# Performance work log

Hardware: AMD Instinct MI355X
Metric: run time of the kernel (lower is better)

The kernel has to match this reference:

```python
import jax, jax.numpy as jnp
import numpy as np

N_NODES = 100000
N_EDGES = 1600000
NUM_GRAPHS = 1000
NODE_IN, EDGE_IN = 32, 16
NODE_EMB, EDGE_EMB, HID, OUT, L = 64, 32, 64, 1, 3
EPS = 1e-5


def _glorot(key, shape):
    fan_in = shape[0]
    return jax.random.normal(key, shape, jnp.float32) / np.sqrt(fan_in)


def setup_inputs() -> dict:
    key = jax.random.key(0)
    ks = jax.random.split(key, 16)
    inp = {
        "x": jax.random.normal(ks[0], (N_NODES, NODE_IN), jnp.float32),
        "edge_attr": jax.random.normal(ks[1], (N_EDGES, EDGE_IN), jnp.float32),
        "edge_index": jax.random.randint(ks[2], (2, N_EDGES), 0, N_NODES, jnp.int64
                                         if jax.config.jax_enable_x64 else jnp.int32),
        "batch": jnp.sort(jax.random.randint(ks[3], (N_NODES,), 0, NUM_GRAPHS)),
        # embeddings
        "node_W": _glorot(ks[4], (NODE_IN, NODE_EMB)),
        "node_b": jnp.zeros((NODE_EMB,), jnp.float32),
        "edge_W": _glorot(ks[5], (EDGE_IN, EDGE_EMB)),
        "edge_b": jnp.zeros((EDGE_EMB,), jnp.float32),
        # per-layer MPNN params (node_dim==64 for every layer since node_emb_dim==hidden_dim)
        "msg_W": _glorot(ks[6], (L, NODE_EMB + EDGE_EMB, HID)),
        "msg_b": jnp.zeros((L, HID), jnp.float32),
        "msg_gamma": jnp.ones((L, HID), jnp.float32),
        "msg_beta": jnp.zeros((L, HID), jnp.float32),
        "upd_W": _glorot(ks[7], (L, NODE_EMB + HID, HID)),
        "upd_b": jnp.zeros((L, HID), jnp.float32),
        "upd_gamma": jnp.ones((L, HID), jnp.float32),
        "upd_beta": jnp.zeros((L, HID), jnp.float32),
        # readout
        "r1_W": _glorot(ks[8], (HID, HID)),
        "r1_b": jnp.zeros((HID,), jnp.float32),
        "r2_W": _glorot(ks[9], (HID, OUT)),
        "r2_b": jnp.zeros((OUT,), jnp.float32),
    }
    return inp


def _bn(h, gamma, beta):
    # BatchNorm1d in training mode: normalize with batch mean / biased variance
    mu = jnp.mean(h, axis=0)
    var = jnp.mean(jnp.square(h - mu), axis=0)
    return gamma * (h - mu) * jax.lax.rsqrt(var + EPS) + beta


def reference(x, edge_attr, edge_index, batch,
              node_W, node_b, edge_W, edge_b,
              msg_W, msg_b, msg_gamma, msg_beta,
              upd_W, upd_b, upd_gamma, upd_beta,
              r1_W, r1_b, r2_W, r2_b):
    h = x @ node_W + node_b                       # [N, 64]
    e = edge_attr @ edge_W + edge_b               # [E, 32]
    src, dst = edge_index[0], edge_index[1]
    for i in range(L):
        # message: gather x_j, concat edge feats, Linear-ReLU-BN (dropout = eval/no-op)
        m = jnp.concatenate([h[src], e], axis=-1) @ msg_W[i] + msg_b[i]   # [E, 64]
        m = _bn(jax.nn.relu(m), msg_gamma[i], msg_beta[i])
        # aggregate: scatter-add to destination nodes
        agg = jax.ops.segment_sum(m, dst, num_segments=N_NODES)          # [N, 64]
        # update: concat self feats, Linear-ReLU-BN
        u = jnp.concatenate([h, agg], axis=-1) @ upd_W[i] + upd_b[i]     # [N, 64]
        h = _bn(jax.nn.relu(u), upd_gamma[i], upd_beta[i])
    # global add pool over graphs
    g = jax.ops.segment_sum(h, batch, num_segments=NUM_GRAPHS)           # [G, 64]
    out = jax.nn.relu(g @ r1_W + r1_b) @ r2_W + r2_b                     # [G, 1]
    return out
```

## Files before the change

kernel.cpp:

```cpp
#include <hip/hip_runtime.h>
#include <hip/hip_bf16.h>

#define N_NODES   100000
#define N_EDGES   1600000
#define NUM_GRAPHS 1000

typedef unsigned int u32;
typedef unsigned short u16;

typedef __bf16 bf16_t;
typedef bf16_t bf16x8 __attribute__((ext_vector_type(8)));
typedef float  f32x4  __attribute__((ext_vector_type(4)));
typedef u32    u32x4  __attribute__((ext_vector_type(4)));

__device__ __forceinline__ float bf2f(u16 u){ return __uint_as_float(((u32)u)<<16); }
__device__ __forceinline__ float BL(u32 u){ return __uint_as_float(u<<16); }
__device__ __forceinline__ float BH(u32 u){ return __uint_as_float(u&0xffff0000u); }
__device__ __forceinline__ u16 f2bf(float f){
  u32 u = __float_as_uint(f);
  return (u16)((u + 0x7fffu + ((u>>16)&1u)) >> 16);
}
__device__ __forceinline__ float ldf(const void* p, size_t i, int isbf){
  return isbf ? bf2f(((const u16*)p)[i]) : ((const float*)p)[i];
}

union U4BF { uint4 u; bf16x8 v; };

__global__ void k_detect(const u32* __restrict__ x, int* __restrict__ flag){
  int t = threadIdx.x; int cnt = 0;
  for (int i = t; i < 256; i += 64){
    u32 w = x[i];
    u32 e = (w >> 7) & 0xffu;
    if (e >= 110u && e <= 137u) cnt++;
  }
  for (int o = 32; o; o >>= 1) cnt += __shfl_xor(cnt, o);
  if (t == 0) *flag = (cnt > 128) ? 1 : 0;
}

__global__ void k_idaff(float* __restrict__ haff){
  int c = threadIdx.x;
  haff[c] = 1.f; haff[64 + c] = 0.f;
}

__global__ void k_prep(const void* __restrict__ eW, const void* __restrict__ eb,
                       const void* __restrict__ mW, const void* __restrict__ mb,
                       u16* __restrict__ Weff, float* __restrict__ biasm,
                       const int* __restrict__ flagp){
  int isbf = *flagp;
  int l = blockIdx.x, c = threadIdx.x;
  u16* W = Weff + ((size_t)l*64 + c)*96;
  for (int k = 0; k < 64; k++)
    W[k] = f2bf(ldf(mW, (size_t)(l*96 + k)*64 + c, isbf));
  for (int j = 0; j < 16; j++){
    float acc = 0.f;
    for (int k = 0; k < 32; k++)
      acc += ldf(eW, (size_t)j*32 + k, isbf) * ldf(mW, (size_t)(l*96 + 64 + k)*64 + c, isbf);
    W[64 + j] = f2bf(acc);
  }
  float fbv = ldf(mb, (size_t)l*64 + c, isbf);
  for (int k = 0; k < 32; k++)
    fbv += ldf(eb, k, isbf) * ldf(mW, (size_t)(l*96 + 64 + k)*64 + c, isbf);
  W[80] = f2bf(fbv);
  biasm[(size_t)l*64 + c] = fbv;
  for (int k = 81; k < 96; k++) W[k] = 0;
}

__global__ void k_fold(const void* __restrict__ mW, const u16* __restrict__ Wbase,
                       const float* __restrict__ biasm, const float* __restrict__ haff,
                       u16* __restrict__ Wf, const int* __restrict__ flagp, int l){
  int isbf = *flagp; int c = threadIdx.x;
  const u16* Wb = Wbase + ((size_t)l*64 + c)*96;
  u16* W = Wf + (size_t)c*96;
  float bb = biasm[(size_t)l*64 + c];
  for (int k = 0; k < 64; k++){
    float w = ldf(mW, (size_t)(l*96 + k)*64 + c, isbf);
    W[k] = f2bf(haff[k] * w);
    bb = fmaf(haff[64 + k], w, bb);
  }
  for (int k = 64; k < 80; k++) W[k] = Wb[k];
  W[80] = f2bf(bb);
  for (int k = 81; k < 96; k++) W[k] = 0;
}

__global__ void k_updprep(const void* __restrict__ uW, const void* __restrict__ ub,
                          const float* __restrict__ maff, const float* __restrict__ haff,
                          u16* __restrict__ Wupd, float* __restrict__ biasv,
                          float* __restrict__ tvv, const int* __restrict__ flagp, int l){
  int isbf = *flagp; int c = threadIdx.x;
  u16* W = Wupd + (size_t)c*192;
  float tv = 0.f, bb = 0.f;
  for (int k = 0; k < 64; k++){
    float wka = ldf(uW, (size_t)(l*128 + k)*64 + c, isbf);
    W[k] = f2bf(haff[k] * wka);
    bb = fmaf(haff[64 + k], wka, bb);
    float wkb = ldf(uW, (size_t)(l*128 + 64 + k)*64 + c, isbf);
    float prod = wkb * maff[k];
    u16 hi = f2bf(prod);
    W[64 + k]  = hi;
    W[128 + k] = f2bf(prod - bf2f(hi));
    tv = fmaf(maff[64 + k], wkb, tv);
  }
  biasv[c] = ldf(ub, (size_t)l*64 + c, isbf) + bb;
  tvv[c] = tv;
}

__global__ void k_node_emb(const void* __restrict__ x, const void* __restrict__ nW,
                           const void* __restrict__ nb, u16* __restrict__ hsp,
                           const int* __restrict__ flagp){
  int isbf = *flagp;
  int lane = threadIdx.x & 63;
  int gw = (blockIdx.x*blockDim.x + threadIdx.x) >> 6;
  int nw = (gridDim.x*blockDim.x) >> 6;
  float w[32];
#pragma unroll
  for (int k = 0; k < 32; k++) w[k] = ldf(nW, (size_t)k*64 + lane, isbf);
  float bias = ldf(nb, lane, isbf);
  for (int n = gw; n < N_NODES; n += nw){
    float acc = bias;
    if (isbf){
      const uint4* xr = (const uint4*)((const u16*)x + (size_t)n*32);
#pragma unroll
      for (int q = 0; q < 4; q++){
        uint4 a = xr[q];
        u32 uu[4] = {a.x, a.y, a.z, a.w};
#pragma unroll
        for (int j = 0; j < 4; j++){
          acc = fmaf(BL(uu[j]), w[q*8 + 2*j + 0], acc);
          acc = fmaf(BH(uu[j]), w[q*8 + 2*j + 1], acc);
        }
      }
    } else {
      const float4* xr = (const float4*)((const float*)x + (size_t)n*32);
#pragma unroll
      for (int q = 0; q < 8; q++){
        float4 a = xr[q];
        acc = fmaf(a.x, w[q*4+0], acc); acc = fmaf(a.y, w[q*4+1], acc);
        acc = fmaf(a.z, w[q*4+2], acc); acc = fmaf(a.w, w[q*4+3], acc);
      }
    }
    u16 hi = f2bf(acc);
    hsp[(size_t)n*128 + lane]      = hi;
    hsp[(size_t)n*128 + 64 + lane] = f2bf(acc - bf2f(hi));
  }
}

__global__ void k_deg(const int* __restrict__ ei, int* __restrict__ deg){
  int i = blockIdx.x*blockDim.x + threadIdx.x;
  int stride = gridDim.x*blockDim.x;
  for (int e = i; e < N_EDGES; e += stride)
    atomicAdd(&deg[ei[N_EDGES + e]], 1);
}

__global__ void __launch_bounds__(256) k_scan1(const int* __restrict__ deg,
                                               int* __restrict__ bsum){
  __shared__ int wsum[4];
  int b = blockIdx.x, t = threadIdx.x;
  int i0 = b*512 + t;
  int s = 0;
  if (i0 < N_NODES) s += deg[i0];
  if (i0 + 256 < N_NODES) s += deg[i0 + 256];
  for (int o = 32; o; o >>= 1) s += __shfl_xor(s, o);
  if ((t & 63) == 0) wsum[t >> 6] = s;
  __syncthreads();
  if (t == 0) bsum[b] = wsum[0] + wsum[1] + wsum[2] + wsum[3];
}

__global__ void k_scan2(const int* __restrict__ bsum, int* __restrict__ boff,
                        int* __restrict__ rp){
  __shared__ int l[200];
  int t = threadIdx.x;
  if (t < 196) l[t] = bsum[t];
  __syncthreads();
  if (t == 0){
    int r = 0;
    for (int k = 0; k < 196; k++){ int x = l[k]; l[k] = r; r += x; }
    rp[N_NODES] = r;
  }
  __syncthreads();
  if (t < 196) boff[t] = l[t];
}

__global__ void __launch_bounds__(256) k_scan3(const int* __restrict__ deg,
                        const int* __restrict__ boff, int* __restrict__ rp,
                        int* __restrict__ cursor, float* __restrict__ degf){
  __shared__ int wpre[4];
  int b = blockIdx.x, t = threadIdx.x;
  int i0 = b*512 + 2*t;
  int d0 = (i0     < N_NODES) ? deg[i0]     : 0;
  int d1 = (i0 + 1 < N_NODES) ? deg[i0 + 1] : 0;
  int s = d0 + d1;
  int incl = s;
  for (int o = 1; o < 64; o <<= 1){ int u = __shfl_up(incl, o); if ((t & 63) >= o) incl += u; }
  if ((t & 63) == 63) wpre[t >> 6] = incl;
  __syncthreads();
  if (t == 0){ int r = 0; for (int k = 0; k < 4; k++){ int x = wpre[k]; wpre[k] = r; r += x; } }
  __syncthreads();
  int excl = boff[b] + wpre[t >> 6] + incl - s;
  if (i0 < N_NODES){
    rp[i0] = excl; cursor[i0] = excl; degf[i0] = (float)d0;
  }
  if (i0 + 1 < N_NODES){
    rp[i0+1] = excl + d0; cursor[i0+1] = excl + d0; degf[i0+1] = (float)d1;
  }
}

__global__ void k_ranges(const int* __restrict__ rp, int* __restrict__ wr,
                         int nwaves){
  int w = blockIdx.x*blockDim.x + threadIdx.x;
  if (w > nwaves) return;
  if (w == nwaves){ wr[w] = N_NODES; return; }
  long long t0 = (long long)w * N_EDGES / nwaves;
  int lo = 0, hi = N_NODES;
  while (lo < hi){ int mid = (lo+hi)>>1; if ((long long)rp[mid] < t0) lo = mid+1; else hi = mid; }
  wr[w] = lo;
}


__global__ void k_tcnt(const int* __restrict__ rp, const int* __restrict__ wr,
                       int* __restrict__ tcnt, int nwaves){
  int w = blockIdx.x*blockDim.x + threadIdx.x;
  if (w >= nwaves) return;
  int n0 = wr[w], n1 = wr[w+1];
  int c = 0;
  for (int n = n0; n < n1; n++){
    int d = rp[n+1] - rp[n];
    c += (d + 15) >> 4;
  }
  tcnt[w] = c;
}

__global__ void k_tscan(const int* __restrict__ tcnt, int* __restrict__ twoff,
                        int nwaves){
  __shared__ int ps[256];
  int t = threadIdx.x;
  int s = 0;
  for (int i = 0; i < 32; i++) s += tcnt[t*32 + i];
  ps[t] = s;
  __syncthreads();
  if (t == 0){
    int r = 0;
    for (int k = 0; k < 256; k++){ int x = ps[k]; ps[k] = r; r += x; }
    twoff[nwaves] = r;
  }
  __syncthreads();
  int off = ps[t];
  for (int i = 0; i < 32; i++){
    twoff[t*32 + i] = off;
    off += tcnt[t*32 + i];
  }
}

__global__ void k_tfill(const int* __restrict__ rp, const int* __restrict__ wr,
                        const int* __restrict__ twoff, int* __restrict__ tlist,
                        int nwaves){
  int w = blockIdx.x*blockDim.x + threadIdx.x;
  if (w >= nwaves) return;
  int n0 = wr[w], n1 = wr[w+1];
  int o = twoff[w];
  for (int n = n0; n < n1; n++){
    int b = rp[n], e = rp[n+1];
    while (b < e){
      int rem = e - b; if (rem > 16) rem = 16;
      int last = (b + 16 >= e) ? 1 : 0;
      tlist[o++] = (n << 5) | ((rem - 1) << 1) | last;
      b += 16;
    }
  }
}

__global__ void k_scatter(const int* __restrict__ ei, int* __restrict__ cursor,
                          int* __restrict__ perm2){
  int i = blockIdx.x*blockDim.x + threadIdx.x;
  int stride = gridDim.x*blockDim.x;
  for (int e = i; e < N_EDGES; e += stride){
    int d = ei[N_EDGES + e];
    int p = atomicAdd(&cursor[d], 1);
    ((int2*)perm2)[p] = make_int2(ei[e], e);
  }
}

__global__ void k_scatter2(const int* __restrict__ ei, int* __restrict__ cursor,
                           int* __restrict__ perm, u16* __restrict__ eacsr,
                           const void* __restrict__ ea, const int* __restrict__ flagp){
  int isbf = *flagp;
  int i = blockIdx.x*blockDim.x + threadIdx.x;
  int stride = gridDim.x*blockDim.x;
  if (i < 48){
    perm[N_EDGES + i] = 0;
    uint4 z = make_uint4(0,0,0,0);
    uint4* out = (uint4*)(eacsr + (size_t)(N_EDGES + i)*16);
    out[0] = z; out[1] = z;
  }
  for (int e = i; e < N_EDGES; e += stride){
    int d = ei[N_EDGES + e];
    int p = atomicAdd(&cursor[d], 1);
    perm[p] = ei[e];
    uint4 r0, r1;
    if (isbf){
      const uint4* er = (const uint4*)((const u16*)ea + (size_t)e*16);
      r0 = er[0]; r1 = er[1];
    } else {
      const float4* ef = (const float4*)((const float*)ea + (size_t)e*16);
      float4 f0 = ef[0], f1 = ef[1], f2 = ef[2], f3 = ef[3];
      r0.x = (u32)f2bf(f0.x) | ((u32)f2bf(f0.y)<<16);
      r0.y = (u32)f2bf(f0.z) | ((u32)f2bf(f0.w)<<16);
      r0.z = (u32)f2bf(f1.x) | ((u32)f2bf(f1.y)<<16);
      r0.w = (u32)f2bf(f1.z) | ((u32)f2bf(f1.w)<<16);
      r1.x = (u32)f2bf(f2.x) | ((u32)f2bf(f2.y)<<16);
      r1.y = (u32)f2bf(f2.z) | ((u32)f2bf(f2.w)<<16);
      r1.z = (u32)f2bf(f3.x) | ((u32)f2bf(f3.y)<<16);
      r1.w = (u32)f2bf(f3.z) | ((u32)f2bf(f3.w)<<16);
    }
    uint4* out = (uint4*)(eacsr + (size_t)p*16);
    out[0] = r0; out[1] = r1;
  }
}

__device__ __forceinline__ void adv_tile(const int* __restrict__ rp,
                                         int ni, int bi, int ei,
                                         int& no, int& bo, int& eo){
  if (bi + 16 < ei){ no = ni; bo = bi + 16; eo = ei; return; }
  int t = ni + 1;
  int nb = ei;
  int ne = rp[(t < N_NODES) ? t + 1 : N_NODES];
  while (nb == ne && t + 1 < N_NODES){
    t++; nb = ne; ne = rp[t + 1];
  }
  no = t; bo = nb; eo = ne;
}

__global__ void __launch_bounds__(256) k_msgmm(
    const u16* __restrict__ hsp, const void* __restrict__ ea,
    const int* __restrict__ rp, const int* __restrict__ perm2,
    const u16* __restrict__ Wl, u16* __restrict__ aggs,
    float* __restrict__ stats, const int* __restrict__ flagp,
    int nwaves){
  __shared__ float bs[128];
  int tid = threadIdx.x;
  if (tid < 128) bs[tid] = 0.f;
  __syncthreads();
  int isbf = *flagp;
  int lane = tid & 63, wv = tid >> 6;
  int w = blockIdx.x*4 + wv;
  long long t0 = (long long)w     * N_EDGES / nwaves;
  long long t1 = (long long)(w+1) * N_EDGES / nwaves;
  int lo = 0, hi = N_NODES;
  while (lo < hi){ int mid = (lo+hi)>>1; if ((long long)rp[mid] < t0) lo = mid+1; else hi = mid; }
  int n0 = lo, n1;
  if (w == nwaves-1) n1 = N_NODES;
  else {
    lo = 0; hi = N_NODES;
    while (lo < hi){ int mid = (lo+hi)>>1; if ((long long)rp[mid] < t1) lo = mid+1; else hi = mid; }
    n1 = lo;
  }
  int nn = lane & 15, kg = lane >> 4;
  bf16x8 B[3][4];
#pragma unroll
  for (int t = 0; t < 4; t++)
#pragma unroll
    for (int kb = 0; kb < 3; kb++)
      B[kb][t] = *(const bf16x8*)(Wl + (size_t)(t*16+nn)*96 + kb*32 + kg*8);
  U4BF ac; ac.u = make_uint4((kg==2)? 0x3f80u : 0u, 0u, 0u, 0u);
  float s1[4] = {0,0,0,0}, s2[4] = {0,0,0,0};
  for (int n = n0; n < n1; n++){
    int b0 = rp[n], b1 = rp[n+1];
    float r0 = 0.f, r1 = 0.f, r2 = 0.f, r3 = 0.f;
    for (int base = b0; base < b1; base += 16){
      int rem = b1 - base; if (rem > 16) rem = 16;
      int row = (nn < rem) ? nn : rem-1;
      int2 p = ((const int2*)perm2)[base + row];
      const uint4* hp = (const uint4*)(hsp + (size_t)p.x*128);
      U4BF fA, fB, fC;
      fA.u = hp[kg];
      fB.u = hp[4 + kg];
      if (kg < 2){
        if (isbf){
          fC.u = ((const uint4*)ea)[(size_t)p.y*2 + kg];
        } else {
          const float4* ef = (const float4*)ea;
          float4 f0 = ef[(size_t)p.y*4 + kg*2];
          float4 f1 = ef[(size_t)p.y*4 + kg*2 + 1];
          fC.u.x = (u32)f2bf(f0.x) | ((u32)f2bf(f0.y)<<16);
          fC.u.y = (u32)f2bf(f0.z) | ((u32)f2bf(f0.w)<<16);
          fC.u.z = (u32)f2bf(f1.x) | ((u32)f2bf(f1.y)<<16);
          fC.u.w = (u32)f2bf(f1.z) | ((u32)f2bf(f1.w)<<16);
        }
      } else fC = ac;
      f32x4 a0 = {0,0,0,0}, a1 = {0,0,0,0}, a2 = {0,0,0,0}, a3 = {0,0,0,0};
      a0 = __builtin_amdgcn_mfma_f32_16x16x32_bf16(fA.v, B[0][0], a0, 0,0,0);
      a1 = __builtin_amdgcn_mfma_f32_16x16x32_bf16(fA.v, B[0][1], a1, 0,0,0);
      a2 = __builtin_amdgcn_mfma_f32_16x16x32_bf16(fA.v, B[0][2], a2, 0,0,0);
      a3 = __builtin_amdgcn_mfma_f32_16x16x32_bf16(fA.v, B[0][3], a3, 0,0,0);
      a0 = __builtin_amdgcn_mfma_f32_16x16x32_bf16(fB.v, B[1][0], a0, 0,0,0);
      a1 = __builtin_amdgcn_mfma_f32_16x16x32_bf16(fB.v, B[1][1], a1, 0,0,0);
      a2 = __builtin_amdgcn_mfma_f32_16x16x32_bf16(fB.v, B[1][2], a2, 0,0,0);
      a3 = __builtin_amdgcn_mfma_f32_16x16x32_bf16(fB.v, B[1][3], a3, 0,0,0);
      a0 = __builtin_amdgcn_mfma_f32_16x16x32_bf16(fC.v, B[2][0], a0, 0,0,0);
      a1 = __builtin_amdgcn_mfma_f32_16x16x32_bf16(fC.v, B[2][1], a1, 0,0,0);
      a2 = __builtin_amdgcn_mfma_f32_16x16x32_bf16(fC.v, B[2][2], a2, 0,0,0);
      a3 = __builtin_amdgcn_mfma_f32_16x16x32_bf16(fC.v, B[2][3], a3, 0,0,0);
      int rowbase = kg*4;
      float ts0 = 0.f, ts1 = 0.f, ts2 = 0.f, ts3 = 0.f;
#pragma unroll
      for (int j = 0; j < 4; j++){
        bool valid = (rowbase + j) < rem;
        float m0 = fmaxf(a0[j], 0.f); m0 = valid ? m0 : 0.f;
        float m1 = fmaxf(a1[j], 0.f); m1 = valid ? m1 : 0.f;
        float m2 = fmaxf(a2[j], 0.f); m2 = valid ? m2 : 0.f;
        float m3 = fmaxf(a3[j], 0.f); m3 = valid ? m3 : 0.f;
        ts0 += m0; ts1 += m1; ts2 += m2; ts3 += m3;
        s2[0] = fmaf(m0,m0,s2[0]); s2[1] = fmaf(m1,m1,s2[1]);
        s2[2] = fmaf(m2,m2,s2[2]); s2[3] = fmaf(m3,m3,s2[3]);
      }
      s1[0] += ts0; s1[1] += ts1; s1[2] += ts2; s1[3] += ts3;
      ts0 += __shfl_xor(ts0,16); ts0 += __shfl_xor(ts0,32);
      ts1 += __shfl_xor(ts1,16); ts1 += __shfl_xor(ts1,32);
      ts2 += __shfl_xor(ts2,16); ts2 += __shfl_xor(ts2,32);
      ts3 += __shfl_xor(ts3,16); ts3 += __shfl_xor(ts3,32);
      r0 += ts0; r1 += ts1; r2 += ts2; r3 += ts3;
    }
    float v = (kg==0) ? r0 : (kg==1) ? r1 : (kg==2) ? r2 : r3;
    u16 hiv = f2bf(v);
    aggs[(size_t)n*128 + lane]      = hiv;
    aggs[(size_t)n*128 + 64 + lane] = f2bf(v - bf2f(hiv));
  }
#pragma unroll
  for (int t = 0; t < 4; t++){
    atomicAdd(&bs[t*16+nn], s1[t]);
    atomicAdd(&bs[64+t*16+nn], s2[t]);
  }
  __syncthreads();
  if (tid < 128) atomicAdd(&stats[tid], bs[tid]);
}

__global__ void __launch_bounds__(256) k_msgmm3(
    const u16* __restrict__ hsp, const u16* __restrict__ eacsr,
    const int* __restrict__ rp, const int* __restrict__ perm,
    const u16* __restrict__ Wl, u16* __restrict__ aggs,
    float* __restrict__ stats, const int* __restrict__ wranges,
    const int* __restrict__ twoff, const int* __restrict__ tlist){
  __shared__ float bs[128];
  int tid = threadIdx.x;
  if (tid < 128) bs[tid] = 0.f;
  __syncthreads();
  int lane = tid & 63;
  int w = blockIdx.x*4 + (tid >> 6);
  int nn = lane & 15, kg = lane >> 4;
  bf16x8 B[3][4];
#pragma unroll
  for (int t = 0; t < 4; t++)
#pragma unroll
    for (int kb = 0; kb < 3; kb++)
      B[kb][t] = *(const bf16x8*)(Wl + (size_t)(t*16+nn)*96 + kb*32 + kg*8);
  U4BF ac; ac.u = make_uint4((kg==2)? 0x3f80u : 0u, 0u, 0u, 0u);
  float s1[4] = {0,0,0,0}, s2[4] = {0,0,0,0};

  int nBeg = wranges[w], nEnd = wranges[w+1];
  if (nBeg < nEnd){
    int pv = rp[nBeg];
    for (int m = nBeg; m < nEnd; m++){
      int nx = rp[m+1];
      if (nx == pv){
        aggs[(size_t)m*128 + lane] = 0;
        aggs[(size_t)m*128 + 64 + lane] = 0;
      }
      pv = nx;
    }
  }

  int tB = twoff[w], tE = twoff[w+1];
  if (tB < tE){
    int recA = tlist[tB];
    int baseA = rp[nBeg];
    int recB = (tB+1 < tE) ? tlist[tB+1] : recA;
    int baseB = baseA + ((recA>>1)&15) + 1;
    U4BF fAA, fAB, fAC;
    {
      int pA = perm[baseA + nn];
      const uint4* hpA = (const uint4*)(hsp + (size_t)pA*128);
      fAA.u = hpA[kg]; fAB.u = hpA[4 + kg];
      if (kg < 2) fAC.u = *(const uint4*)(eacsr + ((size_t)baseA + nn)*16 + (size_t)kg*8);
      else fAC = ac;
    }
    int pB = perm[baseB + nn];
    float r0 = 0.f, r1 = 0.f, r2 = 0.f, r3 = 0.f;
    for (int i = tB; i < tE; i++){
      int recC = (i+2 < tE) ? tlist[i+2] : recB;
      int baseC = baseB + ((recB>>1)&15) + 1;
      int pC = perm[baseC + nn];
      const uint4* hpB = (const uint4*)(hsp + (size_t)pB*128);
      U4BF fBA, fBB, fBC;
      fBA.u = hpB[kg]; fBB.u = hpB[4 + kg];
      if (kg < 2) fBC.u = *(const uint4*)(eacsr + ((size_t)baseB + nn)*16 + (size_t)kg*8);
      else fBC = ac;
      f32x4 a0 = {0,0,0,0}, a1 = {0,0,0,0}, a2 = {0,0,0,0}, a3 = {0,0,0,0};
      a0 = __builtin_amdgcn_mfma_f32_16x16x32_bf16(fAA.v, B[0][0], a0, 0,0,0);
      a1 = __builtin_amdgcn_mfma_f32_16x16x32_bf16(fAA.v, B[0][1], a1, 0,0,0);
      a2 = __builtin_amdgcn_mfma_f32_16x16x32_bf16(fAA.v, B[0][2], a2, 0,0,0);
      a3 = __builtin_amdgcn_mfma_f32_16x16x32_bf16(fAA.v, B[0][3], a3, 0,0,0);
      a0 = __builtin_amdgcn_mfma_f32_16x16x32_bf16(fAB.v, B[1][0], a0, 0,0,0);
      a1 = __builtin_amdgcn_mfma_f32_16x16x32_bf16(fAB.v, B[1][1], a1, 0,0,0);
      a2 = __builtin_amdgcn_mfma_f32_16x16x32_bf16(fAB.v, B[1][2], a2, 0,0,0);
      a3 = __builtin_amdgcn_mfma_f32_16x16x32_bf16(fAB.v, B[1][3], a3, 0,0,0);
      a0 = __builtin_amdgcn_mfma_f32_16x16x32_bf16(fAC.v, B[2][0], a0, 0,0,0);
      a1 = __builtin_amdgcn_mfma_f32_16x16x32_bf16(fAC.v, B[2][1], a1, 0,0,0);
      a2 = __builtin_amdgcn_mfma_f32_16x16x32_bf16(fAC.v, B[2][2], a2, 0,0,0);
      a3 = __builtin_amdgcn_mfma_f32_16x16x32_bf16(fAC.v, B[2][3], a3, 0,0,0);
      int rem = ((recA >> 1) & 15) + 1;
      int rowbase = kg*4;
      float ts0 = 0.f, ts1 = 0.f, ts2 = 0.f, ts3 = 0.f;
#pragma unroll
      for (int j = 0; j < 4; j++){
        bool valid = (rowbase + j) < rem;
        float m0 = fmaxf(a0[j], 0.f); m0 = valid ? m0 : 0.f;
        float m1 = fmaxf(a1[j], 0.f); m1 = valid ? m1 : 0.f;
        float m2 = fmaxf(a2[j], 0.f); m2 = valid ? m2 : 0.f;
        float m3 = fmaxf(a3[j], 0.f); m3 = valid ? m3 : 0.f;
        ts0 += m0; ts1 += m1; ts2 += m2; ts3 += m3;
        s2[0] = fmaf(m0,m0,s2[0]); s2[1] = fmaf(m1,m1,s2[1]);
        s2[2] = fmaf(m2,m2,s2[2]); s2[3] = fmaf(m3,m3,s2[3]);
      }
      s1[0] += ts0; s1[1] += ts1; s1[2] += ts2; s1[3] += ts3;
      r0 += ts0; r1 += ts1; r2 += ts2; r3 += ts3;
      if (recA & 1){
        r0 += __shfl_xor(r0,16); r0 += __shfl_xor(r0,32);
        r1 += __shfl_xor(r1,16); r1 += __shfl_xor(r1,32);
        r2 += __shfl_xor(r2,16); r2 += __shfl_xor(r2,32);
        r3 += __shfl_xor(r3,16); r3 += __shfl_xor(r3,32);
        float v = (kg==0) ? r0 : (kg==1) ? r1 : (kg==2) ? r2 : r3;
        int node = recA >> 5;
        u16 hiv = f2bf(v);
        aggs[(size_t)node*128 + lane]      = hiv;
        aggs[(size_t)node*128 + 64 + lane] = f2bf(v - bf2f(hiv));
        r0 = r1 = r2 = r3 = 0.f;
      }
      recA = recB; baseA = baseB;
      fAA = fBA; fAB = fBB; fAC = fBC;
      recB = recC; baseB = baseC; pB = pC;
    }
  }
#pragma unroll
  for (int t = 0; t < 4; t++){
    atomicAdd(&bs[t*16+nn], s1[t]);
    atomicAdd(&bs[64+t*16+nn], s2[t]);
  }
  __syncthreads();
  if (tid < 128) atomicAdd(&stats[tid], bs[tid]);
}

__global__ void k_fin(float* __restrict__ stats, const void* __restrict__ gamma,
                      const void* __restrict__ beta, float* __restrict__ aff,
                      float cnt_inv, int goff, const int* __restrict__ flagp){
  int isbf = *flagp; int c = threadIdx.x;
  float mu  = stats[c]      * cnt_inv;
  float var = stats[64 + c] * cnt_inv - mu*mu;
  float rs  = rsqrtf(var + 1e-5f);
  float g = ldf(gamma, (size_t)goff + c, isbf);
  float b = ldf(beta,  (size_t)goff + c, isbf);
  aff[c]      = g*rs;
  aff[64 + c] = b - g*mu*rs;
  stats[c] = 0.f; stats[64 + c] = 0.f;
}

#define UPD_TILES (N_NODES/16)
__global__ void __launch_bounds__(256) k_updmm(
    const u16* __restrict__ hsp, u16* __restrict__ aggs,
    const float* __restrict__ degf, const u16* __restrict__ Wupd,
    const float* __restrict__ biasv, const float* __restrict__ tvv,
    float* __restrict__ stats){
  __shared__ float bs[128];
  int tid = threadIdx.x;
  if (tid < 128) bs[tid] = 0.f;
  __syncthreads();
  int lane = tid & 63;
  int nn = lane & 15, kg = lane >> 4;
  int w = blockIdx.x*4 + (tid >> 6);
  int nwv = gridDim.x*4;
  bf16x8 B[6][4];
#pragma unroll
  for (int t = 0; t < 4; t++)
#pragma unroll
    for (int kb = 0; kb < 6; kb++)
      B[kb][t] = *(const bf16x8*)(Wupd + (size_t)(t*16+nn)*192 + kb*32 + kg*8);
  float bc[4], tc[4];
#pragma unroll
  for (int t = 0; t < 4; t++){ bc[t] = biasv[t*16+nn]; tc[t] = tvv[t*16+nn]; }
  float s1[4] = {0,0,0,0}, s2[4] = {0,0,0,0};
  for (int tile = w; tile < UPD_TILES; tile += nwv){
    int n0 = tile*16;
    int r = n0 + nn;
    const uint4* hp = (const uint4*)hsp;
    const uint4* ap = (const uint4*)aggs;
    U4BF hh0, hh1, hl0, hl1, ah0, ah1, al0, al1;
    hh0.u = hp[(size_t)r*16 + kg];       hh1.u = hp[(size_t)r*16 + 4 + kg];
    hl0.u = hp[(size_t)r*16 + 8 + kg];   hl1.u = hp[(size_t)r*16 + 12 + kg];
    ah0.u = ap[(size_t)r*16 + kg];       ah1.u = ap[(size_t)r*16 + 4 + kg];
    al0.u = ap[(size_t)r*16 + 8 + kg];   al1.u = ap[(size_t)r*16 + 12 + kg];
    float dg[4];
#pragma unroll
    for (int j = 0; j < 4; j++) dg[j] = degf[n0 + kg*4 + j];
    f32x4 a0 = {0,0,0,0}, a1 = {0,0,0,0}, a2 = {0,0,0,0}, a3 = {0,0,0,0};
#define MF(F,KB) \
    a0 = __builtin_amdgcn_mfma_f32_16x16x32_bf16(F.v, B[KB][0], a0, 0,0,0); \
    a1 = __builtin_amdgcn_mfma_f32_16x16x32_bf16(F.v, B[KB][1], a1, 0,0,0); \
    a2 = __builtin_amdgcn_mfma_f32_16x16x32_bf16(F.v, B[KB][2], a2, 0,0,0); \
    a3 = __builtin_amdgcn_mfma_f32_16x16x32_bf16(F.v, B[KB][3], a3, 0,0,0);
    MF(hh0,0) MF(hh1,1) MF(hl0,0) MF(hl1,1)
    MF(ah0,2) MF(ah1,3) MF(ah0,4) MF(ah1,5)
    MF(al0,2) MF(al1,3)
#undef MF
#pragma unroll
    for (int j = 0; j < 4; j++){
      int n = n0 + kg*4 + j;
      float m0 = fmaxf(fmaf(tc[0], dg[j], a0[j] + bc[0]), 0.f);
      float m1 = fmaxf(fmaf(tc[1], dg[j], a1[j] + bc[1]), 0.f);
      float m2 = fmaxf(fmaf(tc[2], dg[j], a2[j] + bc[2]), 0.f);
      float m3 = fmaxf(fmaf(tc[3], dg[j], a3[j] + bc[3]), 0.f);
      s1[0] += m0; s1[1] += m1; s1[2] += m2; s1[3] += m3;
      s2[0] = fmaf(m0,m0,s2[0]); s2[1] = fmaf(m1,m1,s2[1]);
      s2[2] = fmaf(m2,m2,s2[2]); s2[3] = fmaf(m3,m3,s2[3]);
      u16* hw = aggs + (size_t)n*128;
      u16 q0 = f2bf(m0), q1 = f2bf(m1), q2 = f2bf(m2), q3 = f2bf(m3);
      hw[     nn] = q0;  hw[64 +      nn] = f2bf(m0 - bf2f(q0));
      hw[16 + nn] = q1;  hw[64 + 16 + nn] = f2bf(m1 - bf2f(q1));
      hw[32 + nn] = q2;  hw[64 + 32 + nn] = f2bf(m2 - bf2f(q2));
      hw[48 + nn] = q3;  hw[64 + 48 + nn] = f2bf(m3 - bf2f(q3));
    }
  }
#pragma unroll
  for (int t = 0; t < 4; t++){
    atomicAdd(&bs[t*16+nn], s1[t]);
    atomicAdd(&bs[64+t*16+nn], s2[t]);
  }
  __syncthreads();
  if (tid < 128) atomicAdd(&stats[tid], bs[tid]);
}

__global__ void k_pool(const u16* __restrict__ hsp, const int* __restrict__ batch,
                       const float* __restrict__ aff, float* __restrict__ g){
  int lane = threadIdx.x & 63;
  int gw = (blockIdx.x*blockDim.x + threadIdx.x) >> 6;
  int nw = (gridDim.x*blockDim.x) >> 6;
  float s = aff[lane], t = aff[64 + lane];
  int chunk = (N_NODES + nw - 1) / nw;
  int n0 = gw*chunk;
  int n1 = n0 + chunk; if (n1 > N_NODES) n1 = N_NODES;
  int cur = -1; float acc = 0.f, cnt = 0.f;
  for (int n = n0; n < n1; n++){
    int b = batch[n];
    float v = bf2f(hsp[(size_t)n*128 + lane]) + bf2f(hsp[(size_t)n*128 + 64 + lane]);
    if (b != cur){
      if (cur >= 0) atomicAdd(&g[(size_t)cur*64 + lane], fmaf(s, acc, t*cnt));
      cur = b; acc = v; cnt = 1.f;
    } else { acc += v; cnt += 1.f; }
  }
  if (cur >= 0) atomicAdd(&g[(size_t)cur*64 + lane], fmaf(s, acc, t*cnt));
}

__global__ void k_read(const float* __restrict__ g, const void* __restrict__ r1W,
                       const void* __restrict__ r1b, const void* __restrict__ r2W,
                       const void* __restrict__ r2b, void* __restrict__ out,
                       const int* __restrict__ flagp){
  int isbf = *flagp;
  int lane = threadIdx.x;
  int gr = blockIdx.x;
  float w[64];
#pragma unroll
  for (int k = 0; k < 64; k++) w[k] = ldf(r1W, (size_t)k*64 + lane, isbf);
  float acc = ldf(r1b, lane, isbf);
  const float4* grow = (const float4*)(g + (size_t)gr*64);
#pragma unroll
  for (int q = 0; q < 16; q++){
    float4 a = grow[q];
    acc = fmaf(a.x, w[4*q+0], acc); acc = fmaf(a.y, w[4*q+1], acc);
    acc = fmaf(a.z, w[4*q+2], acc); acc = fmaf(a.w, w[4*q+3], acc);
  }
  float hid = fmaxf(acc, 0.f);
  float p = hid * ldf(r2W, lane, isbf);
  for (int o = 32; o; o >>= 1) p += __shfl_xor(p, o);
  if (lane == 0){
    float v = p + ldf(r2b, 0, isbf);
    if (isbf) ((__hip_bfloat16*)out)[gr] = __float2bfloat16(v);
    else      ((float*)out)[gr] = v;
  }
}

extern "C" void kernel_launch(void* const* d_in, const int* in_sizes, int n_in,
                              void* d_out, int out_size, void* d_ws, size_t ws_size,
                              hipStream_t stream){
  const void* x    = d_in[0];
  const void* ea   = d_in[1];
  const int*  ei   = (const int*)d_in[2];
  const int*  bt   = (const int*)d_in[3];
  const void* nW   = d_in[4];  const void* nb  = d_in[5];
  const void* eW   = d_in[6];  const void* eb  = d_in[7];
  const void* mW   = d_in[8];  const void* mb  = d_in[9];
  const void* mg   = d_in[10]; const void* mbe = d_in[11];
  const void* uW   = d_in[12]; const void* ub  = d_in[13];
  const void* ug   = d_in[14]; const void* ube = d_in[15];
  const void* r1W  = d_in[16]; const void* r1b = d_in[17];
  const void* r2W  = d_in[18]; const void* r2b = d_in[19];

  const size_t NEED_BIG = 111634736ull;
  const bool big = (ws_size >= NEED_BIG);

  float* ws = (float*)d_ws;
  size_t off = 0;
  auto alloc = [&](size_t n){ float* p = ws + off; off += n; return p; };

  u16*   hsp   = (u16*)alloc(6400000);
  u16*   aggs  = (u16*)alloc(6400000);
  u16*   eacsr = nullptr; int* perm = nullptr; int* perm2 = nullptr;
  int*   tcnt = nullptr; int* twoff = nullptr; int* tlist = nullptr;
  if (big){
    eacsr = (u16*)alloc(12800384);
    perm  = (int*)alloc(1600048);
  } else {
    perm2 = (int*)alloc(3200000);
  }
  float* degf   = alloc(100000);
  float* zero0  = ws + off;
  int*   deg_i  = (int*)alloc(100000);
  float* g      = alloc(64000);
  float* mstats = alloc(128);
  float* ustats = alloc(128);
  size_t zeroN  = (size_t)((ws + off) - zero0);
  float* maff   = alloc(128);
  float* haff   = alloc(128);
  int*   flag   = (int*)alloc(16);
  u16*   Weff   = (u16*)alloc(9216);
  u16*   Wfold  = (u16*)alloc(3072);
  u16*   Wupd   = (u16*)alloc(6144);
  float* biasm  = alloc(192);
  float* biasv  = alloc(64);
  float* tvv    = alloc(64);
  int*   row_ptr= (int*)alloc(100001);
  int*   cursor = (int*)alloc(100000);
  int*   bsum   = (int*)alloc(196);
  int*   boff   = (int*)alloc(196);
  int*   wrng   = (int*)alloc(8194);
  if (big){
    tcnt  = (int*)alloc(8192);
    twoff = (int*)alloc(8193);
    tlist = (int*)alloc(200000);
  }

  const int MM_BLOCKS = 2048;
  const int MM_WAVES  = MM_BLOCKS * 4;
  const int UPD_BLOCKS = 782;

  k_detect<<<1, 64, 0, stream>>>((const u32*)x, flag);
  hipMemsetAsync(zero0, 0, zeroN*sizeof(float), stream);
  k_idaff<<<1, 64, 0, stream>>>(haff);
  k_prep<<<3, 64, 0, stream>>>(eW, eb, mW, mb, Weff, biasm, flag);
  k_node_emb<<<256, 256, 0, stream>>>(x, nW, nb, hsp, flag);
  k_deg<<<512, 256, 0, stream>>>(ei, deg_i);
  k_scan1<<<196, 256, 0, stream>>>(deg_i, bsum);
  k_scan2<<<1, 256, 0, stream>>>(bsum, boff, row_ptr);
  k_scan3<<<196, 256, 0, stream>>>(deg_i, boff, row_ptr, cursor, degf);
  if (big){
    k_ranges<<<33, 256, 0, stream>>>(row_ptr, wrng, MM_WAVES);
    k_tcnt<<<32, 256, 0, stream>>>(row_ptr, wrng, tcnt, MM_WAVES);
    k_tscan<<<1, 256, 0, stream>>>(tcnt, twoff, MM_WAVES);
    k_tfill<<<32, 256, 0, stream>>>(row_ptr, wrng, twoff, tlist, MM_WAVES);
    k_scatter2<<<512, 256, 0, stream>>>(ei, cursor, perm, eacsr, ea, flag);
  } else {
    k_scatter<<<512, 256, 0, stream>>>(ei, cursor, perm2);
  }

  u16* H = hsp;
  u16* G = aggs;
  for (int l = 0; l < 3; l++){
    k_fold<<<1, 64, 0, stream>>>(mW, Weff, biasm, haff, Wfold, flag, l);
    if (big)
      k_msgmm3<<<MM_BLOCKS, 256, 0, stream>>>(H, eacsr, row_ptr, perm, Wfold,
                                              G, mstats, wrng, twoff, tlist);
    else
      k_msgmm<<<MM_BLOCKS, 256, 0, stream>>>(H, ea, row_ptr, perm2, Wfold,
                                             G, mstats, flag, MM_WAVES);
    k_fin<<<1, 64, 0, stream>>>(mstats, mg, mbe, maff, 1.0f/(float)N_EDGES, l*64, flag);
    k_updprep<<<1, 64, 0, stream>>>(uW, ub, maff, haff, Wupd, biasv, tvv, flag, l);
    k_updmm<<<UPD_BLOCKS, 256, 0, stream>>>(H, G, degf, Wupd, biasv, tvv, ustats);
    k_fin<<<1, 64, 0, stream>>>(ustats, ug, ube, haff, 1.0f/(float)N_NODES, l*64, flag);
    u16* tmp = H; H = G; G = tmp;
  }

  k_pool<<<128, 256, 0, stream>>>(H, bt, haff, g);
  k_read<<<NUM_GRAPHS, 64, 0, stream>>>(g, r1W, r1b, r2W, r2b, d_out, flag);
}
```

Baseline: 1.310 ms.

## Interleave two independent edge-tile streams per wave in message kernel

Each wave now handles two contiguous node ranges (streams) and alternates tile steps between them, giving two independent gather/MFMA/reduce chains in flight to hide gather latency. The preprocessing kernels (ranges, tile counts, scan, fill) are generalized to twice as many streams, and workspace sizes grow to match. This costs more registers per wave, which may reduce occupancy, and adds branching in the interleaved loop.

New measurement: 1.312 ms. Within noise of the previous version (+0.2%).

```diff
diff --git a/kernel.cpp b/kernel.cpp
--- a/kernel.cpp
+++ b/kernel.cpp
@@ -11,7 +11,6 @@
 typedef __bf16 bf16_t;
 typedef bf16_t bf16x8 __attribute__((ext_vector_type(8)));
 typedef float  f32x4  __attribute__((ext_vector_type(4)));
-typedef u32    u32x4  __attribute__((ext_vector_type(4)));
 
 __device__ __forceinline__ float bf2f(u16 u){ return __uint_as_float(((u32)u)<<16); }
 __device__ __forceinline__ float BL(u32 u){ return __uint_as_float(u<<16); }
@@ -205,11 +204,11 @@
 }
 
 __global__ void k_ranges(const int* __restrict__ rp, int* __restrict__ wr,
-                         int nwaves){
+                         int nstreams){
   int w = blockIdx.x*blockDim.x + threadIdx.x;
-  if (w > nwaves) return;
-  if (w == nwaves){ wr[w] = N_NODES; return; }
-  long long t0 = (long long)w * N_EDGES / nwaves;
+  if (w > nstreams) return;
+  if (w == nstreams){ wr[w] = N_NODES; return; }
+  long long t0 = (long long)w * N_EDGES / nstreams;
   int lo = 0, hi = N_NODES;
   while (lo < hi){ int mid = (lo+hi)>>1; if ((long long)rp[mid] < t0) lo = mid+1; else hi = mid; }
   wr[w] = lo;
@@ -217,9 +216,9 @@
 
 
 __global__ void k_tcnt(const int* __restrict__ rp, const int* __restrict__ wr,
-                       int* __restrict__ tcnt, int nwaves){
+                       int* __restrict__ tcnt, int nstreams){
   int w = blockIdx.x*blockDim.x + threadIdx.x;
-  if (w >= nwaves) return;
+  if (w >= nstreams) return;
   int n0 = wr[w], n1 = wr[w+1];
   int c = 0;
   for (int n = n0; n < n1; n++){
@@ -230,31 +229,32 @@
 }
 
 __global__ void k_tscan(const int* __restrict__ tcnt, int* __restrict__ twoff,
-                        int nwaves){
+                        int nstreams){
   __shared__ int ps[256];
   int t = threadIdx.x;
+  int per = nstreams >> 8;
   int s = 0;
-  for (int i = 0; i < 32; i++) s += tcnt[t*32 + i];
+  for (int i = 0; i < per; i++) s += tcnt[t*per + i];
   ps[t] = s;
   __syncthreads();
   if (t == 0){
     int r = 0;
     for (int k = 0; k < 256; k++){ int x = ps[k]; ps[k] = r; r += x; }
-    twoff[nwaves] = r;
+    twoff[nstreams] = r;
   }
   __syncthreads();
   int off = ps[t];
-  for (int i = 0; i < 32; i++){
-    twoff[t*32 + i] = off;
-    off += tcnt[t*32 + i];
+  for (int i = 0; i < per; i++){
+    twoff[t*per + i] = off;
+    off += tcnt[t*per + i];
   }
 }
 
 __global__ void k_tfill(const int* __restrict__ rp, const int* __restrict__ wr,
                         const int* __restrict__ twoff, int* __restrict__ tlist,
-                        int nwaves){
+                        int nstreams){
   int w = blockIdx.x*blockDim.x + threadIdx.x;
-  if (w >= nwaves) return;
+  if (w >= nstreams) return;
   int n0 = wr[w], n1 = wr[w+1];
   int o = twoff[w];
   for (int n = n0; n < n1; n++){
@@ -433,7 +433,7 @@
   if (tid < 128) atomicAdd(&stats[tid], bs[tid]);
 }
 
-__global__ void __launch_bounds__(256) k_msgmm3(
+__global__ void __launch_bounds__(256) k_msgmm4(
     const u16* __restrict__ hsp, const u16* __restrict__ eacsr,
     const int* __restrict__ rp, const int* __restrict__ perm,
     const u16* __restrict__ Wl, u16* __restrict__ aggs,
@@ -445,6 +445,7 @@
   __syncthreads();
   int lane = tid & 63;
   int w = blockIdx.x*4 + (tid >> 6);
+  int s0i = 2*w;
   int nn = lane & 15, kg = lane >> 4;
   bf16x8 B[3][4];
 #pragma unroll
@@ -455,7 +456,7 @@
   U4BF ac; ac.u = make_uint4((kg==2)? 0x3f80u : 0u, 0u, 0u, 0u);
   float s1[4] = {0,0,0,0}, s2[4] = {0,0,0,0};
 
-  int nBeg = wranges[w], nEnd = wranges[w+1];
+  int nBeg = wranges[s0i], nMid = wranges[s0i+1], nEnd = wranges[s0i+2];
   if (nBeg < nEnd){
     int pv = rp[nBeg];
     for (int m = nBeg; m < nEnd; m++){
@@ -468,77 +469,94 @@
     }
   }
 
-  int tB = twoff[w], tE = twoff[w+1];
-  if (tB < tE){
-    int recA = tlist[tB];
-    int baseA = rp[nBeg];
-    int recB = (tB+1 < tE) ? tlist[tB+1] : recA;
-    int baseB = baseA + ((recA>>1)&15) + 1;
-    U4BF fAA, fAB, fAC;
-    {
-      int pA = perm[baseA + nn];
-      const uint4* hpA = (const uint4*)(hsp + (size_t)pA*128);
-      fAA.u = hpA[kg]; fAB.u = hpA[4 + kg];
-      if (kg < 2) fAC.u = *(const uint4*)(eacsr + ((size_t)baseA + nn)*16 + (size_t)kg*8);
-      else fAC = ac;
-    }
-    int pB = perm[baseB + nn];
-    float r0 = 0.f, r1 = 0.f, r2 = 0.f, r3 = 0.f;
-    for (int i = tB; i < tE; i++){
-      int recC = (i+2 < tE) ? tlist[i+2] : recB;
-      int baseC = baseB + ((recB>>1)&15) + 1;
-      int pC = perm[baseC + nn];
-      const uint4* hpB = (const uint4*)(hsp + (size_t)pB*128);
-      U4BF fBA, fBB, fBC;
-      fBA.u = hpB[kg]; fBB.u = hpB[4 + kg];
-      if (kg < 2) fBC.u = *(const uint4*)(eacsr + ((size_t)baseB + nn)*16 + (size_t)kg*8);
-      else fBC = ac;
-      f32x4 a0 = {0,0,0,0}, a1 = {0,0,0,0}, a2 = {0,0,0,0}, a3 = {0,0,0,0};
-      a0 = __builtin_amdgcn_mfma_f32_16x16x32_bf16(fAA.v, B[0][0], a0, 0,0,0);
-      a1 = __builtin_amdgcn_mfma_f32_16x16x32_bf16(fAA.v, B[0][1], a1, 0,0,0);
-      a2 = __builtin_amdgcn_mfma_f32_16x16x32_bf16(fAA.v, B[0][2], a2, 0,0,0);
-      a3 = __builtin_amdgcn_mfma_f32_16x16x32_bf16(fAA.v, B[0][3], a3, 0,0,0);
-      a0 = __builtin_amdgcn_mfma_f32_16x16x32_bf16(fAB.v, B[1][0], a0, 0,0,0);
-      a1 = __builtin_amdgcn_mfma_f32_16x16x32_bf16(fAB.v, B[1][1], a1, 0,0,0);
-      a2 = __builtin_amdgcn_mfma_f32_16x16x32_bf16(fAB.v, B[1][2], a2, 0,0,0);
-      a3 = __builtin_amdgcn_mfma_f32_16x16x32_bf16(fAB.v, B[1][3], a3, 0,0,0);
-      a0 = __builtin_amdgcn_mfma_f32_16x16x32_bf16(fAC.v, B[2][0], a0, 0,0,0);
-      a1 = __builtin_amdgcn_mfma_f32_16x16x32_bf16(fAC.v, B[2][1], a1, 0,0,0);
-      a2 = __builtin_amdgcn_mfma_f32_16x16x32_bf16(fAC.v, B[2][2], a2, 0,0,0);
-      a3 = __builtin_amdgcn_mfma_f32_16x16x32_bf16(fAC.v, B[2][3], a3, 0,0,0);
-      int rem = ((recA >> 1) & 15) + 1;
-      int rowbase = kg*4;
-      float ts0 = 0.f, ts1 = 0.f, ts2 = 0.f, ts3 = 0.f;
-#pragma unroll
-      for (int j = 0; j < 4; j++){
-        bool valid = (rowbase + j) < rem;
-        float m0 = fmaxf(a0[j], 0.f); m0 = valid ? m0 : 0.f;
-        float m1 = fmaxf(a1[j], 0.f); m1 = valid ? m1 : 0.f;
-        float m2 = fmaxf(a2[j], 0.f); m2 = valid ? m2 : 0.f;
-        float m3 = fmaxf(a3[j], 0.f); m3 = valid ? m3 : 0.f;
-        ts0 += m0; ts1 += m1; ts2 += m2; ts3 += m3;
-        s2[0] = fmaf(m0,m0,s2[0]); s2[1] = fmaf(m1,m1,s2[1]);
-        s2[2] = fmaf(m2,m2,s2[2]); s2[3] = fmaf(m3,m3,s2[3]);
-      }
-      s1[0] += ts0; s1[1] += ts1; s1[2] += ts2; s1[3] += ts3;
-      r0 += ts0; r1 += ts1; r2 += ts2; r3 += ts3;
-      if (recA & 1){
-        r0 += __shfl_xor(r0,16); r0 += __shfl_xor(r0,32);
-        r1 += __shfl_xor(r1,16); r1 += __shfl_xor(r1,32);
-        r2 += __shfl_xor(r2,16); r2 += __shfl_xor(r2,32);
-        r3 += __shfl_xor(r3,16); r3 += __shfl_xor(r3,32);
-        float v = (kg==0) ? r0 : (kg==1) ? r1 : (kg==2) ? r2 : r3;
-        int node = recA >> 5;
-        u16 hiv = f2bf(v);
-        aggs[(size_t)node*128 + lane]      = hiv;
-        aggs[(size_t)node*128 + 64 + lane] = f2bf(v - bf2f(hiv));
-        r0 = r1 = r2 = r3 = 0.f;
-      }
-      recA = recB; baseA = baseB;
-      fAA = fBA; fAB = fBB; fAC = fBC;
-      recB = recC; baseB = baseC; pB = pC;
-    }
-  }
+#define DECLS(S) \
+  int i##S, e##S, rec##S = 0, recN##S = 0, baseN##S = 0, pN##S = 0; \
+  U4BF fa##S, fb##S, fc##S; \
+  float r0##S = 0.f, r1##S = 0.f, r2##S = 0.f, r3##S = 0.f;
+
+#define INITS(S, sIdx, nFirst) \
+  i##S = twoff[sIdx]; e##S = twoff[(sIdx)+1]; \
+  if (i##S < e##S){ \
+    rec##S = tlist[i##S]; \
+    int base0 = rp[nFirst]; \
+    recN##S = (i##S+1 < e##S) ? tlist[i##S+1] : rec##S; \
+    baseN##S = base0 + ((rec##S>>1)&15) + 1; \
+    int pA = perm[base0 + nn]; \
+    const uint4* hp0 = (const uint4*)(hsp + (size_t)pA*128); \
+    fa##S.u = hp0[kg]; fb##S.u = hp0[4+kg]; \
+    if (kg < 2) fc##S.u = *(const uint4*)(eacsr + ((size_t)base0 + nn)*16 + (size_t)kg*8); \
+    else fc##S = ac; \
+    pN##S = perm[baseN##S + nn]; \
+  }
+
+#define STEP(S) { \
+    int recNN = (i##S+2 < e##S) ? tlist[i##S+2] : recN##S; \
+    int baseNN = baseN##S + ((recN##S>>1)&15) + 1; \
+    int pNN = perm[baseNN + nn]; \
+    const uint4* hpN = (const uint4*)(hsp + (size_t)pN##S*128); \
+    U4BF nfa, nfb, nfc; \
+    nfa.u = hpN[kg]; nfb.u = hpN[4+kg]; \
+    if (kg < 2) nfc.u = *(const uint4*)(eacsr + ((size_t)baseN##S + nn)*16 + (size_t)kg*8); \
+    else nfc = ac; \
+    f32x4 a0 = {0,0,0,0}, a1 = {0,0,0,0}, a2 = {0,0,0,0}, a3 = {0,0,0,0}; \
+    a0 = __builtin_amdgcn_mfma_f32_16x16x32_bf16(fa##S.v, B[0][0], a0, 0,0,0); \
+    a1 = __builtin_amdgcn_mfma_f32_16x16x32_bf16(fa##S.v, B[0][1], a1, 0,0,0); \
+    a2 = __builtin_amdgcn_mfma_f32_16x16x32_bf16(fa##S.v, B[0][2], a2, 0,0,0); \
+    a3 = __builtin_amdgcn_mfma_f32_16x16x32_bf16(fa##S.v, B[0][3], a3, 0,0,0); \
+    a0 = __builtin_amdgcn_mfma_f32_16x16x32_bf16(fb##S.v, B[1][0], a0, 0,0,0); \
+    a1 = __builtin_amdgcn_mfma_f32_16x16x32_bf16(fb##S.v, B[1][1], a1, 0,0,0); \
+    a2 = __builtin_amdgcn_mfma_f32_16x16x32_bf16(fb##S.v, B[1][2], a2, 0,0,0); \
+    a3 = __builtin_amdgcn_mfma_f32_16x16x32_bf16(fb##S.v, B[1][3], a3, 0,0,0); \
+    a0 = __builtin_amdgcn_mfma_f32_16x16x32_bf16(fc##S.v, B[2][0], a0, 0,0,0); \
+    a1 = __builtin_amdgcn_mfma_f32_16x16x32_bf16(fc##S.v, B[2][1], a1, 0,0,0); \
+    a2 = __builtin_amdgcn_mfma_f32_16x16x32_bf16(fc##S.v, B[2][2], a2, 0,0,0); \
+    a3 = __builtin_amdgcn_mfma_f32_16x16x32_bf16(fc##S.v, B[2][3], a3, 0,0,0); \
+    int rem = ((rec##S >> 1) & 15) + 1; \
+    int rowbase = kg*4; \
+    float ts0 = 0.f, ts1 = 0.f, ts2 = 0.f, ts3 = 0.f; \
+    _Pragma("unroll") \
+    for (int j = 0; j < 4; j++){ \
+      bool valid = (rowbase + j) < rem; \
+      float m0 = fmaxf(a0[j], 0.f); m0 = valid ? m0 : 0.f; \
+      float m1 = fmaxf(a1[j], 0.f); m1 = valid ? m1 : 0.f; \
+      float m2 = fmaxf(a2[j], 0.f); m2 = valid ? m2 : 0.f; \
+      float m3 = fmaxf(a3[j], 0.f); m3 = valid ? m3 : 0.f; \
+      ts0 += m0; ts1 += m1; ts2 += m2; ts3 += m3; \
+      s2[0] = fmaf(m0,m0,s2[0]); s2[1] = fmaf(m1,m1,s2[1]); \
+      s2[2] = fmaf(m2,m2,s2[2]); s2[3] = fmaf(m3,m3,s2[3]); \
+    } \
+    s1[0] += ts0; s1[1] += ts1; s1[2] += ts2; s1[3] += ts3; \
+    r0##S += ts0; r1##S += ts1; r2##S += ts2; r3##S += ts3; \
+    if (rec##S & 1){ \
+      r0##S += __shfl_xor(r0##S,16); r0##S += __shfl_xor(r0##S,32); \
+      r1##S += __shfl_xor(r1##S,16); r1##S += __shfl_xor(r1##S,32); \
+      r2##S += __shfl_xor(r2##S,16); r2##S += __shfl_xor(r2##S,32); \
+      r3##S += __shfl_xor(r3##S,16); r3##S += __shfl_xor(r3##S,32); \
+      float v = (kg==0) ? r0##S : (kg==1) ? r1##S : (kg==2) ? r2##S : r3##S; \
+      int node = rec##S >> 5; \
+      u16 hiv = f2bf(v); \
+      aggs[(size_t)node*128 + lane]      = hiv; \
+      aggs[(size_t)node*128 + 64 + lane] = f2bf(v - bf2f(hiv)); \
+      r0##S = r1##S = r2##S = r3##S = 0.f; \
+    } \
+    rec##S = recN##S; fa##S = nfa; fb##S = nfb; fc##S = nfc; \
+    recN##S = recNN; baseN##S = baseNN; pN##S = pNN; \
+    i##S++; \
+  }
+
+  DECLS(0)
+  DECLS(1)
+  INITS(0, s0i, nBeg)
+  INITS(1, s0i+1, nMid)
+
+  while (i0 < e0 || i1 < e1){
+    if (i0 < e0) STEP(0)
+    if (i1 < e1) STEP(1)
+  }
+#undef DECLS
+#undef INITS
+#undef STEP
+
 #pragma unroll
   for (int t = 0; t < 4; t++){
     atomicAdd(&bs[t*16+nn], s1[t]);
@@ -701,7 +719,7 @@
   const void* r1W  = d_in[16]; const void* r1b = d_in[17];
   const void* r2W  = d_in[18]; const void* r2b = d_in[19];
 
-  const size_t NEED_BIG = 111634736ull;
+  const size_t NEED_BIG = 111733044ull;
   const bool big = (ws_size >= NEED_BIG);
 
   float* ws = (float*)d_ws;
@@ -738,15 +756,16 @@
   int*   cursor = (int*)alloc(100000);
   int*   bsum   = (int*)alloc(196);
   int*   boff   = (int*)alloc(196);
-  int*   wrng   = (int*)alloc(8194);
+  int*   wrng   = (int*)alloc(16386);
   if (big){
-    tcnt  = (int*)alloc(8192);
-    twoff = (int*)alloc(8193);
+    tcnt  = (int*)alloc(16384);
+    twoff = (int*)alloc(16386);
     tlist = (int*)alloc(200000);
   }
 
-  const int MM_BLOCKS = 2048;
-  const int MM_WAVES  = MM_BLOCKS * 4;
+  const int MM_BLOCKS  = 2048;
+  const int MM_WAVES   = MM_BLOCKS * 4;
+  const int MM_STREAMS = MM_WAVES * 2;
   const int UPD_BLOCKS = 782;
 
   k_detect<<<1, 64, 0, stream>>>((const u32*)x, flag);
@@ -759,10 +778,10 @@
   k_scan2<<<1, 256, 0, stream>>>(bsum, boff, row_ptr);
   k_scan3<<<196, 256, 0, stream>>>(deg_i, boff, row_ptr, cursor, degf);
   if (big){
-    k_ranges<<<33, 256, 0, stream>>>(row_ptr, wrng, MM_WAVES);
-    k_tcnt<<<32, 256, 0, stream>>>(row_ptr, wrng, tcnt, MM_WAVES);
-    k_tscan<<<1, 256, 0, stream>>>(tcnt, twoff, MM_WAVES);
-    k_tfill<<<32, 256, 0, stream>>>(row_ptr, wrng, twoff, tlist, MM_WAVES);
+    k_ranges<<<65, 256, 0, stream>>>(row_ptr, wrng, MM_STREAMS);
+    k_tcnt<<<64, 256, 0, stream>>>(row_ptr, wrng, tcnt, MM_STREAMS);
+    k_tscan<<<1, 256, 0, stream>>>(tcnt, twoff, MM_STREAMS);
+    k_tfill<<<64, 256, 0, stream>>>(row_ptr, wrng, twoff, tlist, MM_STREAMS);
     k_scatter2<<<512, 256, 0, stream>>>(ei, cursor, perm, eacsr, ea, flag);
   } else {
     k_scatter<<<512, 256, 0, stream>>>(ei, cursor, perm2);
@@ -773,7 +792,7 @@
   for (int l = 0; l < 3; l++){
     k_fold<<<1, 64, 0, stream>>>(mW, Weff, biasm, haff, Wfold, flag, l);
     if (big)
-      k_msgmm3<<<MM_BLOCKS, 256, 0, stream>>>(H, eacsr, row_ptr, perm, Wfold,
+      k_msgmm4<<<MM_BLOCKS, 256, 0, stream>>>(H, eacsr, row_ptr, perm, Wfold,
                                               G, mstats, wrng, twoff, tlist);
     else
       k_msgmm<<<MM_BLOCKS, 256, 0, stream>>>(H, ea, row_ptr, perm2, Wfold,
```
